# Optimization experiments

Hardware: AMD Instinct MI355X
Metric: run time of the kernel (lower is better)

Reference implementation:

```python
import jax, jax.numpy as jnp
import numpy as np

N = 8_388_608   # signal length (2^23 complex samples)
K = 257         # complex filter taps (Savory CD filter)


def setup_inputs() -> dict:
    key = jax.random.key(0)
    k1, k2, k3, k4 = jax.random.split(key, 4)
    return {
        "x_r": jax.random.normal(k1, (N,), jnp.float32),
        "x_i": jax.random.normal(k2, (N,), jnp.float32),
        "w_r": jax.random.normal(k3, (K,), jnp.float32),
        "w_i": jax.random.normal(k4, (K,), jnp.float32),
    }


def reference(x_r, x_i, w_r, w_i):
    # Complex 1D 'full' cross-correlation (torch conv1d with padding = K-1):
    #   y_real = x_r * w_r - x_i * w_i
    #   y_imag = x_i * w_r + x_r * w_i
    # Expressed as a single fused 2-in/2-out real conv (same math as the
    # original 4 separate conv1d calls + elementwise recombine).
    M = w_r.shape[0] - 1
    x = jnp.stack([x_r, x_i])[None]                # [1, 2, N]
    w = jnp.stack([
        jnp.stack([w_r, -w_i]),                    # real output channel
        jnp.stack([w_i,  w_r]),                    # imag output channel
    ])                                             # [2, 2, K]
    y = jax.lax.conv_general_dilated(
        x, w, window_strides=(1,), padding=[(M, M)],
        dimension_numbers=("NCH", "OIH", "NCH"),
    )                                              # [1, 2, N+K-1]
    return y[0]                                    # [2, N+K-1]: row 0 = real, row 1 = imag
```

## Files before the change

### kernel.cpp

```cpp
#include <hip/hip_runtime.h>

typedef _Float16 half8 __attribute__((ext_vector_type(8)));
typedef float    f32x4 __attribute__((ext_vector_type(4)));

#define NLEN   8388608
#define KTAPS  257
#define MPAD   256
#define OUTLEN (NLEN + MPAD)
#define TPB    256
#define BT     4096
#define NBLK   ((OUTLEN + BT - 1) / BT)
#define NCH    9
#define XELEM  (BT + 288)
#define XSLOT  (XELEM / 8)
#define XPAD   556

__device__ __forceinline__ int swz(int t) { return t ^ ((t >> 3) & 7); }

__global__ __launch_bounds__(TPB, 4) void cconv_mfma(
    const float* __restrict__ xr, const float* __restrict__ xi,
    const float* __restrict__ wr, const float* __restrict__ wi,
    float* __restrict__ out)
{
    __shared__ half8 lx[2][XPAD];
    __shared__ half8 af[2][NCH][64];

    const int tid   = threadIdx.x;
    const int wv    = tid >> 6;
    const int lane  = tid & 63;
    const int n15   = lane & 15;
    const int lg    = lane >> 4;
    const int t0    = blockIdx.x * BT;
    const int xbase = t0 - MPAD;

    for (int idx = tid; idx < 2 * NCH * 64; idx += TPB) {
        const int comp = idx / (NCH * 64);
        const int rem  = idx % (NCH * 64);
        const int c    = rem >> 6;
        const int l    = rem & 63;
        const int row  = l & 15;
        const int jb   = 32 * c + 8 * (l >> 4);
        const float* wp = comp ? wi : wr;
        half8 v;
        #pragma unroll
        for (int e = 0; e < 8; ++e) {
            const int k = jb + e - row;
            const float f = (k >= 0 && k < KTAPS) ? wp[k] : 0.0f;
            v[e] = (_Float16)f;
        }
        af[comp][c][l] = v;
    }

    #pragma unroll
    for (int it = 0; it < 3; ++it) {
        const int T = it * TPB + tid;
        if (T < XSLOT) {
            const int g = xbase + 8 * T;
            half8 vr, vi;
            if (g >= 0 && g + 8 <= NLEN) {
                const f32x4 a0 = *(const f32x4*)(xr + g);
                const f32x4 a1 = *(const f32x4*)(xr + g + 4);
                const f32x4 b0 = *(const f32x4*)(xi + g);
                const f32x4 b1 = *(const f32x4*)(xi + g + 4);
                #pragma unroll
                for (int e = 0; e < 4; ++e) {
                    vr[e]     = (_Float16)a0[e];
                    vr[e + 4] = (_Float16)a1[e];
                    vi[e]     = (_Float16)b0[e];
                    vi[e + 4] = (_Float16)b1[e];
                }
            } else {
                #pragma unroll
                for (int e = 0; e < 8; ++e) {
                    const int ge = g + e;
                    const bool ok = (ge >= 0) && (ge < NLEN);
                    vr[e] = (_Float16)(ok ? xr[ge] : 0.0f);
                    vi[e] = (_Float16)(ok ? xi[ge] : 0.0f);
                }
            }
            const int Ts = swz(T);
            lx[0][Ts] = vr;
            lx[1][Ts] = vi;
        }
    }
    __syncthreads();

    f32x4 accr[4], acci[4];
    #pragma unroll
    for (int t = 0; t < 4; ++t) {
        accr[t] = (f32x4)0.0f;
        acci[t] = (f32x4)0.0f;
    }

    const int sT0 = 128 * wv + 2 * n15 + lg;

    #pragma unroll
    for (int c = 0; c < NCH; ++c) {
        const half8 awr = af[0][c][lane];
        const half8 awi = af[1][c][lane];
        #pragma unroll
        for (int t = 0; t < 4; ++t) {
            const int T = sT0 + 32 * t + 4 * c;
            const int Ts = swz(T);
            const half8 br  = lx[0][Ts];
            const half8 bi  = lx[1][Ts];
            const half8 bin = -bi;
            accr[t] = __builtin_amdgcn_mfma_f32_16x16x32_f16(awr, br,  accr[t], 0, 0, 0);
            accr[t] = __builtin_amdgcn_mfma_f32_16x16x32_f16(awi, bin, accr[t], 0, 0, 0);
            acci[t] = __builtin_amdgcn_mfma_f32_16x16x32_f16(awr, bi,  acci[t], 0, 0, 0);
            acci[t] = __builtin_amdgcn_mfma_f32_16x16x32_f16(awi, br,  acci[t], 0, 0, 0);
        }
    }

    const int obase = t0 + 1024 * wv + 16 * n15 + 4 * lg;
    #pragma unroll
    for (int t = 0; t < 4; ++t) {
        const int tbase = t0 + 1024 * wv + 256 * t;
        if (tbase < OUTLEN) {
            const int pos = obase + 256 * t;
            *(f32x4*)(out + pos)          = accr[t];
            *(f32x4*)(out + OUTLEN + pos) = acci[t];
        }
    }
}

extern "C" void kernel_launch(void* const* d_in, const int* in_sizes, int n_in,
                              void* d_out, int out_size, void* d_ws, size_t ws_size,
                              hipStream_t stream) {
    const float* xr = (const float*)d_in[0];
    const float* xi = (const float*)d_in[1];
    const float* wr = (const float*)d_in[2];
    const float* wi = (const float*)d_in[3];
    float* o = (float*)d_out;
    cconv_mfma<<<NBLK, TPB, 0, stream>>>(xr, xi, wr, wi, o);
}
```

Measured before the change: 41.30 us.

## Double block tile, remap blocks across XCDs, split interior loads, use nontemporal stores

Doubles the per-block tile to 8192 outputs with 512 threads, so each block reloads the 256-sample halo less often and the filter-fragment setup is amortized over more work. Block IDs are remapped so each XCD processes a contiguous range of tiles, aiming for better L2 locality between neighbouring halos. Interior blocks use an unconditional vectorized load path, and output writes switch to nontemporal stores to avoid polluting cache. The cost is higher LDS use per block and fewer blocks overall, which may reduce occupancy or hurt tail balance.

```diff
diff --git a/kernel.cpp b/kernel.cpp
--- a/kernel.cpp
+++ b/kernel.cpp
@@ -7,17 +7,18 @@
 #define KTAPS  257
 #define MPAD   256
 #define OUTLEN (NLEN + MPAD)
-#define TPB    256
-#define BT     4096
+#define TPB    512
+#define BT     8192
 #define NBLK   ((OUTLEN + BT - 1) / BT)
 #define NCH    9
 #define XELEM  (BT + 288)
 #define XSLOT  (XELEM / 8)
-#define XPAD   556
+#define XPAD   1068
+#define NXCD   8
 
 __device__ __forceinline__ int swz(int t) { return t ^ ((t >> 3) & 7); }
 
-__global__ __launch_bounds__(TPB, 4) void cconv_mfma(
+__global__ __launch_bounds__(TPB, 6) void cconv_mfma(
     const float* __restrict__ xr, const float* __restrict__ xi,
     const float* __restrict__ wr, const float* __restrict__ wi,
     float* __restrict__ out)
@@ -30,12 +31,18 @@
     const int lane  = tid & 63;
     const int n15   = lane & 15;
     const int lg    = lane >> 4;
-    const int t0    = blockIdx.x * BT;
+
+    const int bidr = blockIdx.x;
+    const int q    = NBLK / NXCD, r = NBLK % NXCD;
+    const int xcd  = bidr % NXCD, idx = bidr / NXCD;
+    const int bid  = (xcd < r ? xcd * (q + 1) : r * (q + 1) + (xcd - r) * q) + idx;
+
+    const int t0    = bid * BT;
     const int xbase = t0 - MPAD;
 
-    for (int idx = tid; idx < 2 * NCH * 64; idx += TPB) {
-        const int comp = idx / (NCH * 64);
-        const int rem  = idx % (NCH * 64);
+    for (int i = tid; i < 2 * NCH * 64; i += TPB) {
+        const int comp = i / (NCH * 64);
+        const int rem  = i % (NCH * 64);
         const int c    = rem >> 6;
         const int l    = rem & 63;
         const int row  = l & 15;
@@ -51,36 +58,40 @@
         af[comp][c][l] = v;
     }
 
-    #pragma unroll
-    for (int it = 0; it < 3; ++it) {
-        const int T = it * TPB + tid;
-        if (T < XSLOT) {
+    const bool interior = (xbase >= 0) && (xbase + 8 * XSLOT <= NLEN);
+    if (interior) {
+        for (int T = tid; T < XSLOT; T += TPB) {
             const int g = xbase + 8 * T;
-            half8 vr, vi;
-            if (g >= 0 && g + 8 <= NLEN) {
-                const f32x4 a0 = *(const f32x4*)(xr + g);
-                const f32x4 a1 = *(const f32x4*)(xr + g + 4);
-                const f32x4 b0 = *(const f32x4*)(xi + g);
-                const f32x4 b1 = *(const f32x4*)(xi + g + 4);
-                #pragma unroll
-                for (int e = 0; e < 4; ++e) {
-                    vr[e]     = (_Float16)a0[e];
-                    vr[e + 4] = (_Float16)a1[e];
-                    vi[e]     = (_Float16)b0[e];
-                    vi[e + 4] = (_Float16)b1[e];
-                }
-            } else {
-                #pragma unroll
-                for (int e = 0; e < 8; ++e) {
-                    const int ge = g + e;
-                    const bool ok = (ge >= 0) && (ge < NLEN);
-                    vr[e] = (_Float16)(ok ? xr[ge] : 0.0f);
-                    vi[e] = (_Float16)(ok ? xi[ge] : 0.0f);
-                }
+            const f32x4 a0 = *(const f32x4*)(xr + g);
+            const f32x4 a1 = *(const f32x4*)(xr + g + 4);
+            const f32x4 b0 = *(const f32x4*)(xi + g);
+            const f32x4 b1 = *(const f32x4*)(xi + g + 4);
+            half8 vrr, vii;
+            #pragma unroll
+            for (int e = 0; e < 4; ++e) {
+                vrr[e]     = (_Float16)a0[e];
+                vrr[e + 4] = (_Float16)a1[e];
+                vii[e]     = (_Float16)b0[e];
+                vii[e + 4] = (_Float16)b1[e];
             }
             const int Ts = swz(T);
-            lx[0][Ts] = vr;
-            lx[1][Ts] = vi;
+            lx[0][Ts] = vrr;
+            lx[1][Ts] = vii;
+        }
+    } else {
+        for (int T = tid; T < XSLOT; T += TPB) {
+            const int g = xbase + 8 * T;
+            half8 vrr, vii;
+            #pragma unroll
+            for (int e = 0; e < 8; ++e) {
+                const int ge = g + e;
+                const bool ok = (ge >= 0) && (ge < NLEN);
+                vrr[e] = (_Float16)(ok ? xr[ge] : 0.0f);
+                vii[e] = (_Float16)(ok ? xi[ge] : 0.0f);
+            }
+            const int Ts = swz(T);
+            lx[0][Ts] = vrr;
+            lx[1][Ts] = vii;
         }
     }
     __syncthreads();
@@ -100,7 +111,7 @@
         const half8 awi = af[1][c][lane];
         #pragma unroll
         for (int t = 0; t < 4; ++t) {
-            const int T = sT0 + 32 * t + 4 * c;
+            const int T  = sT0 + 32 * t + 4 * c;
             const int Ts = swz(T);
             const half8 br  = lx[0][Ts];
             const half8 bi  = lx[1][Ts];
@@ -118,8 +129,8 @@
         const int tbase = t0 + 1024 * wv + 256 * t;
         if (tbase < OUTLEN) {
             const int pos = obase + 256 * t;
-            *(f32x4*)(out + pos)          = accr[t];
-            *(f32x4*)(out + OUTLEN + pos) = acci[t];
+            __builtin_nontemporal_store(accr[t], (f32x4*)(out + pos));
+            __builtin_nontemporal_store(acci[t], (f32x4*)(out + OUTLEN + pos));
         }
     }
 }
```

After: 47.90 us. +16.0%, slower.

## Precompute filter fragments once in workspace and read them from global memory

Applied to the files above, without the earlier changes.

Adds a single-block prep kernel that builds the fp16 Toeplitz weight fragments into the workspace buffer. The main kernel then reads them from global/L2 with software prefetch instead of every block rebuilding them in LDS. This removes the per-block weight construction and frees LDS, and launch bounds are raised to allow 8 blocks per CU. The weight negation moves from the activation to the filter fragment once per chunk, and staging gets a branch-free interior path. The cost is an extra kernel launch, plus weight fragments now come from cache rather than LDS; a fallback kernel is kept for when no workspace is available.

```diff
diff --git a/kernel.cpp b/kernel.cpp
--- a/kernel.cpp
+++ b/kernel.cpp
@@ -14,16 +14,80 @@
 #define XELEM  (BT + 288)
 #define XSLOT  (XELEM / 8)
 #define XPAD   556
+#define AFSLOT (2 * NCH * 64)
 
 __device__ __forceinline__ int swz(int t) { return t ^ ((t >> 3) & 7); }
 
-__global__ __launch_bounds__(TPB, 4) void cconv_mfma(
+__device__ __forceinline__ void stage_x(const float* __restrict__ xr,
+                                        const float* __restrict__ xi,
+                                        half8 (*lx)[XPAD], int xbase, int tid)
+{
+    const bool interior = (xbase >= 0) && (xbase + 8 * XSLOT <= NLEN);
+    if (interior) {
+        for (int T = tid; T < XSLOT; T += TPB) {
+            const int g = xbase + 8 * T;
+            const f32x4 a0 = *(const f32x4*)(xr + g);
+            const f32x4 a1 = *(const f32x4*)(xr + g + 4);
+            const f32x4 b0 = *(const f32x4*)(xi + g);
+            const f32x4 b1 = *(const f32x4*)(xi + g + 4);
+            half8 vr, vi;
+            #pragma unroll
+            for (int e = 0; e < 4; ++e) {
+                vr[e]     = (_Float16)a0[e];
+                vr[e + 4] = (_Float16)a1[e];
+                vi[e]     = (_Float16)b0[e];
+                vi[e + 4] = (_Float16)b1[e];
+            }
+            const int Ts = swz(T);
+            lx[0][Ts] = vr;
+            lx[1][Ts] = vi;
+        }
+    } else {
+        for (int T = tid; T < XSLOT; T += TPB) {
+            const int g = xbase + 8 * T;
+            half8 vr, vi;
+            #pragma unroll
+            for (int e = 0; e < 8; ++e) {
+                const int ge = g + e;
+                const bool ok = (ge >= 0) && (ge < NLEN);
+                vr[e] = (_Float16)(ok ? xr[ge] : 0.0f);
+                vi[e] = (_Float16)(ok ? xi[ge] : 0.0f);
+            }
+            const int Ts = swz(T);
+            lx[0][Ts] = vr;
+            lx[1][Ts] = vi;
+        }
+    }
+}
+
+__global__ __launch_bounds__(TPB) void build_af(
+    const float* __restrict__ wr, const float* __restrict__ wi,
+    half8* __restrict__ af)
+{
+    for (int i = threadIdx.x; i < AFSLOT; i += TPB) {
+        const int comp = i / (NCH * 64);
+        const int rem  = i % (NCH * 64);
+        const int c    = rem >> 6;
+        const int l    = rem & 63;
+        const int row  = l & 15;
+        const int jb   = 32 * c + 8 * (l >> 4);
+        const float* wp = comp ? wi : wr;
+        half8 v;
+        #pragma unroll
+        for (int e = 0; e < 8; ++e) {
+            const int k = jb + e - row;
+            const float f = (k >= 0 && k < KTAPS) ? wp[k] : 0.0f;
+            v[e] = (_Float16)f;
+        }
+        af[i] = v;
+    }
+}
+
+__global__ __launch_bounds__(TPB, 8) void cconv_ws(
     const float* __restrict__ xr, const float* __restrict__ xi,
-    const float* __restrict__ wr, const float* __restrict__ wi,
-    float* __restrict__ out)
+    const half8* __restrict__ af, float* __restrict__ out)
 {
     __shared__ half8 lx[2][XPAD];
-    __shared__ half8 af[2][NCH][64];
 
     const int tid   = threadIdx.x;
     const int wv    = tid >> 6;
@@ -33,9 +97,68 @@
     const int t0    = blockIdx.x * BT;
     const int xbase = t0 - MPAD;
 
-    for (int idx = tid; idx < 2 * NCH * 64; idx += TPB) {
-        const int comp = idx / (NCH * 64);
-        const int rem  = idx % (NCH * 64);
+    stage_x(xr, xi, lx, xbase, tid);
+    __syncthreads();
+
+    f32x4 accr[4], acci[4];
+    #pragma unroll
+    for (int t = 0; t < 4; ++t) { accr[t] = (f32x4)0.0f; acci[t] = (f32x4)0.0f; }
+
+    const int sT0 = 128 * wv + 2 * n15 + lg;
+    const half8* afr = af + lane;
+    const half8* afi = af + NCH * 64 + lane;
+
+    half8 awr = afr[0];
+    half8 awi = afi[0];
+    for (int c = 0; c < NCH; ++c) {
+        const int cn = (c + 1 < NCH) ? c + 1 : 0;
+        const half8 nwr = afr[cn * 64];
+        const half8 nwi = afi[cn * 64];
+        const half8 awin = -awi;
+        #pragma unroll
+        for (int t = 0; t < 4; ++t) {
+            const int Ts = swz(sT0 + 32 * t + 4 * c);
+            const half8 br = lx[0][Ts];
+            const half8 bi = lx[1][Ts];
+            accr[t] = __builtin_amdgcn_mfma_f32_16x16x32_f16(awr,  br, accr[t], 0, 0, 0);
+            accr[t] = __builtin_amdgcn_mfma_f32_16x16x32_f16(awin, bi, accr[t], 0, 0, 0);
+            acci[t] = __builtin_amdgcn_mfma_f32_16x16x32_f16(awr,  bi, acci[t], 0, 0, 0);
+            acci[t] = __builtin_amdgcn_mfma_f32_16x16x32_f16(awi,  br, acci[t], 0, 0, 0);
+        }
+        awr = nwr; awi = nwi;
+    }
+
+    const int obase = t0 + 1024 * wv + 16 * n15 + 4 * lg;
+    #pragma unroll
+    for (int t = 0; t < 4; ++t) {
+        const int tbase = t0 + 1024 * wv + 256 * t;
+        if (tbase < OUTLEN) {
+            const int pos = obase + 256 * t;
+            *(f32x4*)(out + pos)          = accr[t];
+            *(f32x4*)(out + OUTLEN + pos) = acci[t];
+        }
+    }
+}
+
+__global__ __launch_bounds__(TPB, 4) void cconv_local(
+    const float* __restrict__ xr, const float* __restrict__ xi,
+    const float* __restrict__ wr, const float* __restrict__ wi,
+    float* __restrict__ out)
+{
+    __shared__ half8 lx[2][XPAD];
+    __shared__ half8 af[2][NCH][64];
+
+    const int tid   = threadIdx.x;
+    const int wv    = tid >> 6;
+    const int lane  = tid & 63;
+    const int n15   = lane & 15;
+    const int lg    = lane >> 4;
+    const int t0    = blockIdx.x * BT;
+    const int xbase = t0 - MPAD;
+
+    for (int i = tid; i < AFSLOT; i += TPB) {
+        const int comp = i / (NCH * 64);
+        const int rem  = i % (NCH * 64);
         const int c    = rem >> 6;
         const int l    = rem & 63;
         const int row  = l & 15;
@@ -50,65 +173,29 @@
         }
         af[comp][c][l] = v;
     }
-
-    #pragma unroll
-    for (int it = 0; it < 3; ++it) {
-        const int T = it * TPB + tid;
-        if (T < XSLOT) {
-            const int g = xbase + 8 * T;
-            half8 vr, vi;
-            if (g >= 0 && g + 8 <= NLEN) {
-                const f32x4 a0 = *(const f32x4*)(xr + g);
-                const f32x4 a1 = *(const f32x4*)(xr + g + 4);
-                const f32x4 b0 = *(const f32x4*)(xi + g);
-                const f32x4 b1 = *(const f32x4*)(xi + g + 4);
-                #pragma unroll
-                for (int e = 0; e < 4; ++e) {
-                    vr[e]     = (_Float16)a0[e];
-                    vr[e + 4] = (_Float16)a1[e];
-                    vi[e]     = (_Float16)b0[e];
-                    vi[e + 4] = (_Float16)b1[e];
-                }
-            } else {
-                #pragma unroll
-                for (int e = 0; e < 8; ++e) {
-                    const int ge = g + e;
-                    const bool ok = (ge >= 0) && (ge < NLEN);
-                    vr[e] = (_Float16)(ok ? xr[ge] : 0.0f);
-                    vi[e] = (_Float16)(ok ? xi[ge] : 0.0f);
-                }
-            }
-            const int Ts = swz(T);
-            lx[0][Ts] = vr;
-            lx[1][Ts] = vi;
-        }
-    }
+    stage_x(xr, xi, lx, xbase, tid);
     __syncthreads();
 
     f32x4 accr[4], acci[4];
     #pragma unroll
-    for (int t = 0; t < 4; ++t) {
-        accr[t] = (f32x4)0.0f;
-        acci[t] = (f32x4)0.0f;
-    }
+    for (int t = 0; t < 4; ++t) { accr[t] = (f32x4)0.0f; acci[t] = (f32x4)0.0f; }
 
     const int sT0 = 128 * wv + 2 * n15 + lg;
 
     #pragma unroll
     for (int c = 0; c < NCH; ++c) {
-        const half8 awr = af[0][c][lane];
-        const half8 awi = af[1][c][lane];
+        const half8 awr  = af[0][c][lane];
+        const half8 awi  = af[1][c][lane];
+        const half8 awin = -awi;
         #pragma unroll
         for (int t = 0; t < 4; ++t) {
-            const int T = sT0 + 32 * t + 4 * c;
-            const int Ts = swz(T);
-            const half8 br  = lx[0][Ts];
-            const half8 bi  = lx[1][Ts];
-            const half8 bin = -bi;
-            accr[t] = __builtin_amdgcn_mfma_f32_16x16x32_f16(awr, br,  accr[t], 0, 0, 0);
-            accr[t] = __builtin_amdgcn_mfma_f32_16x16x32_f16(awi, bin, accr[t], 0, 0, 0);
-            acci[t] = __builtin_amdgcn_mfma_f32_16x16x32_f16(awr, bi,  acci[t], 0, 0, 0);
-            acci[t] = __builtin_amdgcn_mfma_f32_16x16x32_f16(awi, br,  acci[t], 0, 0, 0);
+            const int Ts = swz(sT0 + 32 * t + 4 * c);
+            const half8 br = lx[0][Ts];
+            const half8 bi = lx[1][Ts];
+            accr[t] = __builtin_amdgcn_mfma_f32_16x16x32_f16(awr,  br, accr[t], 0, 0, 0);
+            accr[t] = __builtin_amdgcn_mfma_f32_16x16x32_f16(awin, bi, accr[t], 0, 0, 0);
+            acci[t] = __builtin_amdgcn_mfma_f32_16x16x32_f16(awr,  bi, acci[t], 0, 0, 0);
+            acci[t] = __builtin_amdgcn_mfma_f32_16x16x32_f16(awi,  br, acci[t], 0, 0, 0);
         }
     }
 
@@ -132,5 +219,10 @@
     const float* wr = (const float*)d_in[2];
     const float* wi = (const float*)d_in[3];
     float* o = (float*)d_out;
-    cconv_mfma<<<NBLK, TPB, 0, stream>>>(xr, xi, wr, wi, o);
-}
+    if (ws_size >= (size_t)AFSLOT * 16) {
+        build_af<<<1, TPB, 0, stream>>>(wr, wi, (half8*)d_ws);
+        cconv_ws<<<NBLK, TPB, 0, stream>>>(xr, xi, (const half8*)d_ws, o);
+    } else {
+        cconv_local<<<NBLK, TPB, 0, stream>>>(xr, xi, wr, wi, o);
+    }
+}
```

After: 79.20 us. 1.92x slower.
